# Kernel tuning notes

Hardware: AMD Instinct MI355X
Metric: run time of the kernel (lower is better)

Reference implementation:

```python
import jax, jax.numpy as jnp
import numpy as np

N, E, IN_DIM, OUT_DIM, N_GRAPHS = 50000, 400000, 64, 128, 64


def setup_inputs() -> dict:
    key = jax.random.key(0)
    ks = jax.random.split(key, 16)
    x = jax.random.normal(ks[0], (N, IN_DIM), dtype=jnp.float32)
    edge_index = jax.random.randint(ks[1], (2, E), 0, N, dtype=jnp.int32)
    batch = jnp.sort(jax.random.randint(ks[2], (N,), 0, N_GRAPHS, dtype=jnp.int32))

    def glorot(k, shape):
        lim = np.sqrt(6.0 / (shape[0] + shape[1]))
        return jax.random.uniform(k, shape, jnp.float32, -lim, lim)

    d = IN_DIM
    return {
        "x": x, "edge_index": edge_index, "batch": batch,
        "W1": glorot(ks[3], (d, 2 * d)),     "b1": jnp.zeros((2 * d,), jnp.float32),
        "W2": glorot(ks[4], (2 * d, 4 * d)), "b2": jnp.zeros((4 * d,), jnp.float32),
        "W3": glorot(ks[5], (d, 2 * d)),     "b3": jnp.zeros((2 * d,), jnp.float32),
        "W4": glorot(ks[6], (2 * d, 4 * d)), "b4": jnp.zeros((4 * d,), jnp.float32),
        "W7": glorot(ks[7], (9 * d, OUT_DIM)), "b7": jnp.zeros((OUT_DIM,), jnp.float32),
    }


def _gcn_conv(x, W, b, src, dst, dis):
    # GCNConv: x' = D^{-1/2} (A + I) D^{-1/2} (x W) + b
    h = x @ W                                   # [N, F]
    norm = dis[src] * dis[dst]                  # [E]
    agg = jax.ops.segment_sum(h[src] * norm[:, None], dst, num_segments=N)
    agg = agg + h * (dis * dis)[:, None]        # self-loop contribution
    return agg + b


def reference(x, edge_index, batch, W1, b1, W2, b2, W3, b3, W4, b4, W7, b7):
    src, dst = edge_index[0], edge_index[1]
    # degree of A + I (PyG counts in-degree over columns, +1 for self-loop)
    deg = jax.ops.segment_sum(jnp.ones((E,), x.dtype), dst, num_segments=N) + 1.0
    dis = jax.lax.rsqrt(deg)

    i1 = jnp.tanh(_gcn_conv(x, W1, b1, src, dst, dis))
    i1 = jnp.tanh(_gcn_conv(i1, W2, b2, src, dst, dis))
    i1 = jax.ops.segment_max(i1, batch, num_segments=N_GRAPHS)  # global_max_pool
    i1 = jnp.max(i1, axis=0, keepdims=True)                     # [1, 4d]
    i1 = jnp.broadcast_to(i1, (x.shape[0], i1.shape[1]))        # expand to [N, 4d]

    i2 = jnp.tanh(_gcn_conv(x, W3, b3, src, dst, dis))
    i2 = jnp.tanh(_gcn_conv(i2, W4, b4, src, dst, dis))

    c = jnp.concatenate((i1, i2, x), axis=1)                    # [N, 9d]
    return jnp.tanh(_gcn_conv(c, W7, b7, src, dst, dis))
```

## Files before the change

kernel.cpp:

```cpp
#include <hip/hip_runtime.h>
#include <hip/hip_bf16.h>
#include <cstdint>
#include <cstddef>

#define NN 50000
#define EE 400000

typedef __attribute__((ext_vector_type(8))) __bf16 bf16x8;
typedef __attribute__((ext_vector_type(4))) float f32x4;

static __device__ __forceinline__ float dec_key(unsigned k) {
  return (k & 0x80000000u) ? __uint_as_float(k & 0x7fffffffu) : __uint_as_float(~k);
}
static __device__ __forceinline__ unsigned enc_key(float f) {
  unsigned b = __float_as_uint(f);
  return (f >= 0.f) ? (b | 0x80000000u) : ~b;
}

__global__ void count_kernel(const int* __restrict__ dst, int* __restrict__ cnt, int e) {
  int i = blockIdx.x * blockDim.x + threadIdx.x;
  if (i < e) atomicAdd(&cnt[dst[i]], 1);
}

__global__ void dis_kernel(const int* __restrict__ cnt, float* __restrict__ dis, int n) {
  int i = blockIdx.x * blockDim.x + threadIdx.x;
  if (i < n) dis[i] = rsqrtf((float)cnt[i] + 1.0f);
}

#define SCAN_CHUNK 1024
__global__ __launch_bounds__(256) void scan1_kernel(const int* __restrict__ cnt,
                                                    int* __restrict__ rowptr,
                                                    int* __restrict__ bsum, int n) {
  int b = blockIdx.x;
  int base = b * SCAN_CHUNK;
  int t = threadIdx.x;
  int v[4];
  int s = 0;
#pragma unroll
  for (int i = 0; i < 4; ++i) {
    int idx = base + t * 4 + i;
    v[i] = (idx < n) ? cnt[idx] : 0;
    s += v[i];
  }
  int lane = t & 63, w = t >> 6;
  int inc = s;
#pragma unroll
  for (int off = 1; off < 64; off <<= 1) {
    int o = __shfl_up(inc, off, 64);
    if (lane >= off) inc += o;
  }
  __shared__ int wsum[4];
  if (lane == 63) wsum[w] = inc;
  __syncthreads();
  int woff = 0;
  for (int i = 0; i < w; ++i) woff += wsum[i];
  int run = woff + inc - s;
#pragma unroll
  for (int i = 0; i < 4; ++i) {
    int idx = base + t * 4 + i;
    if (idx < n) rowptr[idx] = run;
    run += v[i];
  }
  if (t == 255) bsum[b] = woff + inc;
}

__global__ void scan2_kernel(int* __restrict__ bsum, int nb) {
  int t = threadIdx.x;
  int v = (t < nb) ? bsum[t] : 0;
  int s = v;
#pragma unroll
  for (int off = 1; off < 64; off <<= 1) {
    int o = __shfl_up(s, off, 64);
    if (t >= off) s += o;
  }
  if (t < nb) bsum[t] = s - v;
}

__global__ __launch_bounds__(256) void scan3_kernel(int* __restrict__ rowptr,
                                                    const int* __restrict__ bsum, int n, int total) {
  int i = blockIdx.x * blockDim.x + threadIdx.x;
  if (i < n) rowptr[i] += bsum[i >> 10];
  if (i == 0) rowptr[n] = total;
}

__global__ void fill_kernel(const int* __restrict__ src, const int* __restrict__ dst,
                            const int* __restrict__ rowptr, int* __restrict__ cursor,
                            int* __restrict__ col, int e) {
  int i = blockIdx.x * blockDim.x + threadIdx.x;
  if (i < e) {
    int d = dst[i];
    int p = atomicAdd(&cursor[d], 1);
    col[rowptr[d] + p] = src[i];
  }
}

#define BM 64
#define BN 64
#define BK 16

__global__ __launch_bounds__(256) void gemm_f32(
    const float* __restrict__ A, const float* __restrict__ W, float* __restrict__ C,
    int M, int K, int Nout, const float* __restrict__ colAdd, int accumulate, int doTanh) {
  __shared__ float As[BK][BM + 4];
  __shared__ float Ws[BK][BN];
  int tid = threadIdx.x;
  int row0 = blockIdx.x * BM;
  int col0 = blockIdx.y * BN;
  int tx = tid & 15;
  int ty = tid >> 4;
  float acc[4][4] = {};
  for (int k0 = 0; k0 < K; k0 += BK) {
#pragma unroll
    for (int i = 0; i < 4; ++i) {
      int idx = tid + i * 256;
      int r = idx >> 4, c = idx & 15;
      int gr = row0 + r;
      float v = (gr < M) ? A[(size_t)gr * K + k0 + c] : 0.f;
      As[c][r] = v;
    }
#pragma unroll
    for (int i = 0; i < 4; ++i) {
      int idx = tid + i * 256;
      int r = idx >> 6, c = idx & 63;
      Ws[r][c] = W[(size_t)(k0 + r) * Nout + col0 + c];
    }
    __syncthreads();
#pragma unroll
    for (int kk = 0; kk < BK; ++kk) {
      float4 av = *(const float4*)&As[kk][ty * 4];
      float4 wv = *(const float4*)&Ws[kk][tx * 4];
      float a[4] = {av.x, av.y, av.z, av.w};
      float w[4] = {wv.x, wv.y, wv.z, wv.w};
#pragma unroll
      for (int i = 0; i < 4; ++i)
#pragma unroll
        for (int j = 0; j < 4; ++j) acc[i][j] = fmaf(a[i], w[j], acc[i][j]);
    }
    __syncthreads();
  }
#pragma unroll
  for (int i = 0; i < 4; ++i) {
    int gr = row0 + ty * 4 + i;
    if (gr >= M) continue;
#pragma unroll
    for (int j = 0; j < 4; ++j) {
      int gc = col0 + tx * 4 + j;
      size_t idx = (size_t)gr * Nout + gc;
      float v = acc[i][j];
      if (colAdd) v += colAdd[gc];
      if (accumulate) v += C[idx];
      if (doTanh) v = tanhf(v);
      C[idx] = v;
    }
  }
}

#define TM 128
#define TN 64
#define TK 64

__global__ __launch_bounds__(256) void gemm_mfma(
    const float* __restrict__ A, const float* __restrict__ W, float* __restrict__ C,
    int M, int K, int Nout, const float* __restrict__ colAdd, int accumulate, int doTanh,
    unsigned* __restrict__ colmaxOut) {
  __shared__ char lds[(TM * TK + TN * TK) * 2];
  char* AsB = lds;
  char* BtB = lds + TM * TK * 2;
  int tid = threadIdx.x;
  int row0 = blockIdx.x * TM;
  int col0 = blockIdx.y * TN;
  int w = tid >> 6, l = tid & 63;
  int lr = l & 15, lh = l >> 4;
  int wmB = (w >> 1) * 64;
  int wnB = (w & 1) * 32;
  f32x4 acc[4][2] = {};
  for (int k0 = 0; k0 < K; k0 += TK) {
    if (k0) __syncthreads();
#pragma unroll
    for (int i = 0; i < 4; ++i) {
      int id = tid + i * 256;
      int r = id >> 3, oc = id & 7;
      int gr = row0 + r;
      float f[8];
      if (gr < M) {
        const float* ga = A + (size_t)gr * K + k0 + oc * 8;
        f32x4 v0 = *(const f32x4*)ga;
        f32x4 v1 = *(const f32x4*)(ga + 4);
        f[0] = v0.x; f[1] = v0.y; f[2] = v0.z; f[3] = v0.w;
        f[4] = v1.x; f[5] = v1.y; f[6] = v1.z; f[7] = v1.w;
      } else {
#pragma unroll
        for (int j = 0; j < 8; ++j) f[j] = 0.f;
      }
      bf16x8 sv;
#pragma unroll
      for (int j = 0; j < 8; ++j) sv[j] = (__bf16)f[j];
      int byte = (r * 128 + oc * 16) ^ ((r & 7) << 4);
      *(bf16x8*)(AsB + byte) = sv;
    }
#pragma unroll
    for (int i = 0; i < 2; ++i) {
      int id = tid + i * 256;
      int c = id & 63, ko = id >> 6;
      const float* gw = W + (size_t)(k0 + ko * 8) * Nout + col0 + c;
      bf16x8 sv;
#pragma unroll
      for (int j = 0; j < 8; ++j) sv[j] = (__bf16)gw[(size_t)j * Nout];
      int byte = (c * 128 + ko * 16) ^ ((c & 7) << 4);
      *(bf16x8*)(BtB + byte) = sv;
    }
    __syncthreads();
#pragma unroll
    for (int s = 0; s < 2; ++s) {
      bf16x8 af[4], bfr[2];
#pragma unroll
      for (int mi = 0; mi < 4; ++mi) {
        int r = wmB + mi * 16 + lr;
        int byte = (r * 128 + (s * 32 + lh * 8) * 2) ^ ((r & 7) << 4);
        af[mi] = *(const bf16x8*)(AsB + byte);
      }
#pragma unroll
      for (int ni = 0; ni < 2; ++ni) {
        int c = wnB + ni * 16 + lr;
        int byte = (c * 128 + (s * 32 + lh * 8) * 2) ^ ((c & 7) << 4);
        bfr[ni] = *(const bf16x8*)(BtB + byte);
      }
#pragma unroll
      for (int mi = 0; mi < 4; ++mi)
#pragma unroll
        for (int ni = 0; ni < 2; ++ni)
          acc[mi][ni] =
              __builtin_amdgcn_mfma_f32_16x16x32_bf16(af[mi], bfr[ni], acc[mi][ni], 0, 0, 0);
    }
  }
  float cmax[2] = {-2.0f, -2.0f};
#pragma unroll
  for (int mi = 0; mi < 4; ++mi) {
#pragma unroll
    for (int ni = 0; ni < 2; ++ni) {
#pragma unroll
      for (int r = 0; r < 4; ++r) {
        int gr = row0 + wmB + mi * 16 + lh * 4 + r;
        if (gr >= M) continue;
        int gc = col0 + wnB + ni * 16 + lr;
        size_t idx = (size_t)gr * Nout + gc;
        float v = acc[mi][ni][r];
        if (colAdd) v += colAdd[gc];
        if (accumulate) v += C[idx];
        if (doTanh) v = tanhf(v);
        if (colmaxOut) cmax[ni] = fmaxf(cmax[ni], v);
        C[idx] = v;
      }
    }
  }
  if (colmaxOut) {
#pragma unroll
    for (int ni = 0; ni < 2; ++ni) {
      float m = cmax[ni];
      m = fmaxf(m, __shfl_xor(m, 16));
      m = fmaxf(m, __shfl_xor(m, 32));
      if (lh == 0) {
        int gc = col0 + wnB + ni * 16 + lr;
        atomicMax(&colmaxOut[gc], enc_key(m));
      }
    }
  }
}

template <int F, bool EPI>
__global__ __launch_bounds__(256) void agg_kernel(
    const float* __restrict__ H, const int* __restrict__ rowptr, const int* __restrict__ col,
    const float* __restrict__ dis, const float* __restrict__ bias, float* __restrict__ out, int n) {
  constexpr int VEC = F / 64;
  int wid = (int)((blockIdx.x * blockDim.x + threadIdx.x) >> 6);
  int lane = threadIdx.x & 63;
  if (wid >= n) return;
  int node = __builtin_amdgcn_readfirstlane(wid);
  float dd = dis[node];
  float acc[VEC];
  {
    const float* hs = H + (size_t)node * F + lane * VEC;
    if constexpr (VEC == 4) {
      float4 h = *(const float4*)hs;
      acc[0] = h.x * dd * dd; acc[1] = h.y * dd * dd; acc[2] = h.z * dd * dd; acc[3] = h.w * dd * dd;
    } else if constexpr (VEC == 2) {
      float2 h = *(const float2*)hs;
      acc[0] = h.x * dd * dd; acc[1] = h.y * dd * dd;
    } else {
      acc[0] = hs[0] * dd * dd;
    }
  }
  int beg = rowptr[node], end = rowptr[node + 1];
  for (int e = beg; e < end; ++e) {
    int s = col[e];
    float w = dis[s] * dd;
    const float* hs = H + (size_t)s * F + lane * VEC;
    if constexpr (VEC == 4) {
      float4 h = *(const float4*)hs;
      acc[0] = fmaf(h.x, w, acc[0]); acc[1] = fmaf(h.y, w, acc[1]);
      acc[2] = fmaf(h.z, w, acc[2]); acc[3] = fmaf(h.w, w, acc[3]);
    } else if constexpr (VEC == 2) {
      float2 h = *(const float2*)hs;
      acc[0] = fmaf(h.x, w, acc[0]); acc[1] = fmaf(h.y, w, acc[1]);
    } else {
      acc[0] = fmaf(hs[0], w, acc[0]);
    }
  }
  float* o = out + (size_t)node * F + lane * VEC;
#pragma unroll
  for (int i = 0; i < VEC; ++i) {
    float v = acc[i];
    if constexpr (EPI) v = tanhf(v + bias[lane * VEC + i]);
    o[i] = v;
  }
}

__global__ __launch_bounds__(128) void crow_kernel(const unsigned* __restrict__ maxkey,
                                                   const float* __restrict__ W7top,
                                                   float* __restrict__ crow) {
  int j = threadIdx.x;
  float s = 0.f;
  for (int f = 0; f < 256; ++f) s = fmaf(dec_key(maxkey[f]), W7top[f * 128 + j], s);
  crow[j] = s;
}

extern "C" void kernel_launch(void* const* d_in, const int* in_sizes, int n_in,
                              void* d_out, int out_size, void* d_ws, size_t ws_size,
                              hipStream_t stream) {
  const float* x  = (const float*)d_in[0];
  const int* ei   = (const int*)d_in[1];
  const int* srcp = ei;
  const int* dstp = ei + EE;
  const float* W1 = (const float*)d_in[3];
  const float* b1 = (const float*)d_in[4];
  const float* W2 = (const float*)d_in[5];
  const float* b2 = (const float*)d_in[6];
  const float* W3 = (const float*)d_in[7];
  const float* b3 = (const float*)d_in[8];
  const float* W4 = (const float*)d_in[9];
  const float* b4 = (const float*)d_in[10];
  const float* W7 = (const float*)d_in[11];
  const float* b7 = (const float*)d_in[12];
  float* out = (float*)d_out;

  char* p = (char*)d_ws;
  auto alloc = [&](size_t bytes) -> void* {
    void* r = (void*)p;
    p += (bytes + 255) & ~(size_t)255;
    return r;
  };
  float* H  = (float*)alloc((size_t)NN * 256 * 4);
  float* A  = (float*)alloc((size_t)NN * 128 * 4);
  float* B  = (float*)alloc((size_t)NN * 256 * 4);
  float* AX = (float*)alloc((size_t)NN * 64 * 4);
  float* dis = (float*)alloc((size_t)NN * 4);
  int* cnt = (int*)alloc((size_t)NN * 4);
  int* cursor = (int*)alloc((size_t)NN * 4);
  int* rowptr = (int*)alloc((size_t)(NN + 1) * 4);
  int* col = (int*)alloc((size_t)EE * 4);
  int* bsum = (int*)alloc(64 * 4);
  unsigned* maxkey = (unsigned*)alloc(256 * 4);
  float* crow = (float*)alloc(128 * 4);

  hipMemsetAsync(cnt, 0, (size_t)NN * 4, stream);
  hipMemsetAsync(cursor, 0, (size_t)NN * 4, stream);
  hipMemsetAsync(maxkey, 0, 256 * 4, stream);

  int eb = (EE + 255) / 256;
  int nb = (NN + 255) / 256;
  int nchunks = (NN + SCAN_CHUNK - 1) / SCAN_CHUNK;
  count_kernel<<<eb, 256, 0, stream>>>(dstp, cnt, EE);
  dis_kernel<<<nb, 256, 0, stream>>>(cnt, dis, NN);
  scan1_kernel<<<nchunks, 256, 0, stream>>>(cnt, rowptr, bsum, NN);
  scan2_kernel<<<1, 64, 0, stream>>>(bsum, nchunks);
  scan3_kernel<<<nb, 256, 0, stream>>>(rowptr, bsum, NN, EE);
  fill_kernel<<<eb, 256, 0, stream>>>(srcp, dstp, rowptr, cursor, col, EE);

  dim3 gB(256);
  int mrows = (NN + BM - 1) / BM;
  int mrowsT = (NN + TM - 1) / TM;
  int aggB = (NN + 3) / 4;

  agg_kernel<64, false><<<aggB, gB, 0, stream>>>(x, rowptr, col, dis, nullptr, AX, NN);
  gemm_f32<<<dim3(mrows, 2), gB, 0, stream>>>(AX, W1, A, NN, 64, 128, b1, 0, 1);
  agg_kernel<128, false><<<aggB, gB, 0, stream>>>(A, rowptr, col, dis, nullptr, H, NN);
  gemm_mfma<<<dim3(mrowsT, 4), gB, 0, stream>>>(H, W2, B, NN, 128, 256, b2, 0, 1, maxkey);
  gemm_f32<<<dim3(mrows, 2), gB, 0, stream>>>(AX, W3, A, NN, 64, 128, b3, 0, 1);
  agg_kernel<128, false><<<aggB, gB, 0, stream>>>(A, rowptr, col, dis, nullptr, H, NN);
  gemm_mfma<<<dim3(mrowsT, 4), gB, 0, stream>>>(H, W4, B, NN, 128, 256, b4, 0, 1, nullptr);
  crow_kernel<<<1, 128, 0, stream>>>(maxkey, W7, crow);
  gemm_mfma<<<dim3(mrowsT, 2), gB, 0, stream>>>(B, W7 + 256 * 128, H, NN, 256, 128, crow, 0, 0, nullptr);
  gemm_f32<<<dim3(mrows, 2), gB, 0, stream>>>(x, W7 + 512 * 128, H, NN, 64, 128, nullptr, 1, 0);
  agg_kernel<128, true><<<aggB, gB, 0, stream>>>(H, rowptr, col, dis, b7, out, NN);
}
```

Before: 495.9 us.

## Store MFMA GEMM operands as bf16 and pre-transpose weights

Aggregation outputs that feed the MFMA GEMMs are now written as bf16, and the layer-4 GEMM writes its output in bf16 for the final GEMM. Weights are converted once into transposed bf16 copies by a small kernel, so GEMM tile loads become contiguous 16-byte vector loads with no in-kernel conversion. The layer-2 GEMM no longer stores its output at all, because only its column max is needed. This halves intermediate memory traffic and removes strided weight loads, at the cost of three extra small launches and bf16 rounding of stored intermediates (previously rounding happened only inside the GEMM).

```diff
diff --git a/kernel.cpp b/kernel.cpp
--- a/kernel.cpp
+++ b/kernel.cpp
@@ -91,6 +91,15 @@
     int d = dst[i];
     int p = atomicAdd(&cursor[d], 1);
     col[rowptr[d] + p] = src[i];
+  }
+}
+
+__global__ __launch_bounds__(256) void wcvt_kernel(const float* __restrict__ W,
+                                                   __bf16* __restrict__ Wt, int K, int Nout) {
+  int idx = blockIdx.x * blockDim.x + threadIdx.x;
+  if (idx < K * Nout) {
+    int n = idx / K, k = idx - n * K;
+    Wt[idx] = (__bf16)W[(size_t)k * Nout + n];
   }
 }
 
@@ -160,8 +169,9 @@
 #define TK 64
 
 __global__ __launch_bounds__(256) void gemm_mfma(
-    const float* __restrict__ A, const float* __restrict__ W, float* __restrict__ C,
-    int M, int K, int Nout, const float* __restrict__ colAdd, int accumulate, int doTanh,
+    const __bf16* __restrict__ A, const __bf16* __restrict__ Wt,
+    float* __restrict__ Cf, __bf16* __restrict__ Ch,
+    int M, int K, int Nout, const float* __restrict__ colAdd, int doTanh,
     unsigned* __restrict__ colmaxOut) {
   __shared__ char lds[(TM * TK + TN * TK) * 2];
   char* AsB = lds;
@@ -181,32 +191,18 @@
       int id = tid + i * 256;
       int r = id >> 3, oc = id & 7;
       int gr = row0 + r;
-      float f[8];
-      if (gr < M) {
-        const float* ga = A + (size_t)gr * K + k0 + oc * 8;
-        f32x4 v0 = *(const f32x4*)ga;
-        f32x4 v1 = *(const f32x4*)(ga + 4);
-        f[0] = v0.x; f[1] = v0.y; f[2] = v0.z; f[3] = v0.w;
-        f[4] = v1.x; f[5] = v1.y; f[6] = v1.z; f[7] = v1.w;
-      } else {
-#pragma unroll
-        for (int j = 0; j < 8; ++j) f[j] = 0.f;
-      }
       bf16x8 sv;
-#pragma unroll
-      for (int j = 0; j < 8; ++j) sv[j] = (__bf16)f[j];
+      if (gr < M) sv = *(const bf16x8*)(A + (size_t)gr * K + k0 + oc * 8);
+      else sv = bf16x8{};
       int byte = (r * 128 + oc * 16) ^ ((r & 7) << 4);
       *(bf16x8*)(AsB + byte) = sv;
     }
 #pragma unroll
     for (int i = 0; i < 2; ++i) {
       int id = tid + i * 256;
-      int c = id & 63, ko = id >> 6;
-      const float* gw = W + (size_t)(k0 + ko * 8) * Nout + col0 + c;
-      bf16x8 sv;
-#pragma unroll
-      for (int j = 0; j < 8; ++j) sv[j] = (__bf16)gw[(size_t)j * Nout];
-      int byte = (c * 128 + ko * 16) ^ ((c & 7) << 4);
+      int c = id >> 3, oc = id & 7;
+      bf16x8 sv = *(const bf16x8*)(Wt + (size_t)(col0 + c) * K + k0 + oc * 8);
+      int byte = (c * 128 + oc * 16) ^ ((c & 7) << 4);
       *(bf16x8*)(BtB + byte) = sv;
     }
     __syncthreads();
@@ -246,10 +242,10 @@
         size_t idx = (size_t)gr * Nout + gc;
         float v = acc[mi][ni][r];
         if (colAdd) v += colAdd[gc];
-        if (accumulate) v += C[idx];
         if (doTanh) v = tanhf(v);
         if (colmaxOut) cmax[ni] = fmaxf(cmax[ni], v);
-        C[idx] = v;
+        if (Cf) Cf[idx] = v;
+        if (Ch) Ch[idx] = (__bf16)v;
       }
     }
   }
@@ -267,10 +263,10 @@
   }
 }
 
-template <int F, bool EPI>
+template <int F, bool EPI, typename OT>
 __global__ __launch_bounds__(256) void agg_kernel(
     const float* __restrict__ H, const int* __restrict__ rowptr, const int* __restrict__ col,
-    const float* __restrict__ dis, const float* __restrict__ bias, float* __restrict__ out, int n) {
+    const float* __restrict__ dis, const float* __restrict__ bias, OT* __restrict__ out, int n) {
   constexpr int VEC = F / 64;
   int wid = (int)((blockIdx.x * blockDim.x + threadIdx.x) >> 6);
   int lane = threadIdx.x & 63;
@@ -306,12 +302,12 @@
       acc[0] = fmaf(hs[0], w, acc[0]);
     }
   }
-  float* o = out + (size_t)node * F + lane * VEC;
+  OT* o = out + (size_t)node * F + lane * VEC;
 #pragma unroll
   for (int i = 0; i < VEC; ++i) {
     float v = acc[i];
     if constexpr (EPI) v = tanhf(v + bias[lane * VEC + i]);
-    o[i] = v;
+    o[i] = (OT)v;
   }
 }
 
@@ -349,10 +345,14 @@
     p += (bytes + 255) & ~(size_t)255;
     return r;
   };
-  float* H  = (float*)alloc((size_t)NN * 256 * 4);
-  float* A  = (float*)alloc((size_t)NN * 128 * 4);
-  float* B  = (float*)alloc((size_t)NN * 256 * 4);
-  float* AX = (float*)alloc((size_t)NN * 64 * 4);
+  float*  H   = (float*)alloc((size_t)NN * 128 * 4);
+  float*  A   = (float*)alloc((size_t)NN * 128 * 4);
+  __bf16* Hb  = (__bf16*)alloc((size_t)NN * 128 * 2);
+  __bf16* Bb  = (__bf16*)alloc((size_t)NN * 256 * 2);
+  float*  AX  = (float*)alloc((size_t)NN * 64 * 4);
+  __bf16* W2t = (__bf16*)alloc((size_t)256 * 128 * 2);
+  __bf16* W4t = (__bf16*)alloc((size_t)256 * 128 * 2);
+  __bf16* W7t = (__bf16*)alloc((size_t)128 * 256 * 2);
   float* dis = (float*)alloc((size_t)NN * 4);
   int* cnt = (int*)alloc((size_t)NN * 4);
   int* cursor = (int*)alloc((size_t)NN * 4);
@@ -376,20 +376,24 @@
   scan3_kernel<<<nb, 256, 0, stream>>>(rowptr, bsum, NN, EE);
   fill_kernel<<<eb, 256, 0, stream>>>(srcp, dstp, rowptr, cursor, col, EE);
 
+  wcvt_kernel<<<(256 * 128 + 255) / 256, 256, 0, stream>>>(W2, W2t, 128, 256);
+  wcvt_kernel<<<(256 * 128 + 255) / 256, 256, 0, stream>>>(W4, W4t, 128, 256);
+  wcvt_kernel<<<(128 * 256 + 255) / 256, 256, 0, stream>>>(W7 + 256 * 128, W7t, 256, 128);
+
   dim3 gB(256);
   int mrows = (NN + BM - 1) / BM;
   int mrowsT = (NN + TM - 1) / TM;
   int aggB = (NN + 3) / 4;
 
-  agg_kernel<64, false><<<aggB, gB, 0, stream>>>(x, rowptr, col, dis, nullptr, AX, NN);
+  agg_kernel<64, false, float><<<aggB, gB, 0, stream>>>(x, rowptr, col, dis, nullptr, AX, NN);
   gemm_f32<<<dim3(mrows, 2), gB, 0, stream>>>(AX, W1, A, NN, 64, 128, b1, 0, 1);
-  agg_kernel<128, false><<<aggB, gB, 0, stream>>>(A, rowptr, col, dis, nullptr, H, NN);
-  gemm_mfma<<<dim3(mrowsT, 4), gB, 0, stream>>>(H, W2, B, NN, 128, 256, b2, 0, 1, maxkey);
+  agg_kernel<128, false, __bf16><<<aggB, gB, 0, stream>>>(A, rowptr, col, dis, nullptr, Hb, NN);
+  gemm_mfma<<<dim3(mrowsT, 4), gB, 0, stream>>>(Hb, W2t, nullptr, nullptr, NN, 128, 256, b2, 1, maxkey);
   gemm_f32<<<dim3(mrows, 2), gB, 0, stream>>>(AX, W3, A, NN, 64, 128, b3, 0, 1);
-  agg_kernel<128, false><<<aggB, gB, 0, stream>>>(A, rowptr, col, dis, nullptr, H, NN);
-  gemm_mfma<<<dim3(mrowsT, 4), gB, 0, stream>>>(H, W4, B, NN, 128, 256, b4, 0, 1, nullptr);
+  agg_kernel<128, false, __bf16><<<aggB, gB, 0, stream>>>(A, rowptr, col, dis, nullptr, Hb, NN);
+  gemm_mfma<<<dim3(mrowsT, 4), gB, 0, stream>>>(Hb, W4t, nullptr, Bb, NN, 128, 256, b4, 1, nullptr);
   crow_kernel<<<1, 128, 0, stream>>>(maxkey, W7, crow);
-  gemm_mfma<<<dim3(mrowsT, 2), gB, 0, stream>>>(B, W7 + 256 * 128, H, NN, 256, 128, crow, 0, 0, nullptr);
+  gemm_mfma<<<dim3(mrowsT, 2), gB, 0, stream>>>(Bb, W7t, H, nullptr, NN, 256, 128, crow, 0, nullptr);
   gemm_f32<<<dim3(mrows, 2), gB, 0, stream>>>(x, W7 + 512 * 128, H, NN, 64, 128, nullptr, 1, 0);
-  agg_kernel<128, true><<<aggB, gB, 0, stream>>>(H, rowptr, col, dis, b7, out, NN);
-}
+  agg_kernel<128, true, float><<<aggB, gB, 0, stream>>>(H, rowptr, col, dis, b7, out, NN);
+}
```

Measured after the change: 477.4 us. 3.7% less time.
